# Optimization experiments

Hardware: AMD Instinct MI355X
Metric: run time of the kernel (lower is better)

The kernel has to match this reference:

```python
import jax, jax.numpy as jnp
import numpy as np

TEMP = 100.0          # config.networks.pseudo_temp
THRESH2 = 100.0 ** 2  # config.networks.keypoint_loss.error_thresh ** 2
NEG = -1e30


def se3_inv(T):
    R, t = T[:3, :3], T[:3, 3]
    return jnp.eye(4, dtype=T.dtype).at[:3, :3].set(R.T).at[:3, 3].set(-R.T @ t)


def convert_weight_mat(w):
    # w: [N,6] -> Wmat = L diag(exp(d)) L^T  (unit lower-triangular L), d = w[:,3:6]
    N = w.shape[0]
    d = w[:, 3:6]
    L = jnp.tile(jnp.eye(3, dtype=w.dtype), (N, 1, 1))
    L = L.at[:, 1, 0].set(w[:, 0]).at[:, 2, 0].set(w[:, 1]).at[:, 2, 1].set(w[:, 2])
    Wmat = jnp.einsum('nij,nj,nkj->nik', L, jnp.exp(d), L)
    return Wmat, d


def _pair_loss(src, tgt, w, m1, m2, wv, T_src, T_tgt):
    # src,tgt: [3,N]; w: [6,N]; m1,m2: [N] bool masks (ragged nonzero -> masking); wv: [N,N]
    N = wv.shape[0]
    points1 = src.T                                   # [N,3]
    w12c = jnp.where(m2[None, :], wv, NEG)            # mask invalid tgt columns
    soft = jax.nn.softmax(w12c * TEMP, axis=1)        # pseudo-correspondence weights
    points2 = soft @ tgt.T                            # [N,3] pseudo points
    Wmat, d = convert_weight_mat(w.T)                 # [N,3,3], [N,3]
    # match consistency (argmax in both directions over valid rows/cols)
    ind2to1 = jnp.argmax(w12c, axis=1)
    ind1to2 = jnp.argmax(jnp.where(m1[:, None], wv, NEG), axis=0)
    consist = ind1to2[ind2to1] == jnp.arange(N)
    mask = m1 & consist
    # groundtruth relative transform, transport points1 into frame 2
    T21 = se3_inv(T_tgt) @ T_src
    p1in2 = points1 @ T21[:3, :3].T + T21[:3, 3][None, :]
    e = p1in2 - points2                               # steam_pseudo: points2e == points2
    mah = jnp.einsum('ni,nij,nj->n', e, Wmat, e)      # Mahalanobis error
    inlier = (mask & (mah < THRESH2)).astype(mah.dtype)
    cnt = jnp.maximum(inlier.sum(), 1.0)
    # weighted MSE (mean of e^T W e over inliers) minus mean log-det reward
    return (mah * inlier).sum() / cnt - (d.sum(1) * inlier).sum() / cnt


def setup_inputs() -> dict:
    key = jax.random.key(0)
    ks = jax.random.split(key, 6)
    B, N = 4, 5760
    return {
        'src_coords': jax.random.normal(ks[0], (B, 3, N), jnp.float32),
        'tgt_coords': jax.random.normal(ks[1], (B, 3, N), jnp.float32),
        'weights':    jax.random.normal(ks[2], (B, 6, N), jnp.float32),
        'match_vals': jax.random.normal(ks[3], (B, N, N), jnp.float32),
        'T_iv':       jax.random.normal(ks[4], (2 * B, 4, 4), jnp.float32),
        'patch_mask': jax.random.randint(ks[5], (2 * B, N), 0, 2, jnp.int32),
    }


def reference(src_coords, tgt_coords, weights, match_vals, T_iv, patch_mask):
    m = patch_mask.astype(bool)
    losses = jax.vmap(_pair_loss)(
        src_coords, tgt_coords, weights,
        m[0::2], m[1::2], match_vals, T_iv[0::2], T_iv[1::2])
    return losses.sum()
```

## Files before the change

kernel.cpp:

```cpp
#include <hip/hip_runtime.h>
#include <stdint.h>

#define TEMP_F 100.0f
#define NEG_F (-1e30f)
#define THRESH2_F 10000.0f

typedef unsigned long long ull;

__device__ __forceinline__ ull packvi(float v, int idx) {
    unsigned u = __float_as_uint(v);
    u = (u & 0x80000000u) ? ~u : (u | 0x80000000u);
    return (((ull)u) << 32) | (ull)(0xFFFFFFFFu - (unsigned)idx);
}
__device__ __forceinline__ float unpackv(ull p) {
    unsigned u = (unsigned)(p >> 32);
    u = (u & 0x80000000u) ? (u & 0x7FFFFFFFu) : ~u;
    return __uint_as_float(u);
}
__device__ __forceinline__ ull u64max(ull a, ull b) { return a > b ? a : b; }

__global__ void init_kernel(const float* __restrict__ Tiv,
                            ull* __restrict__ colPacked,
                            float* __restrict__ acc, float* __restrict__ T21,
                            int* __restrict__ validCnt,
                            int B, int N) {
    int idx = blockIdx.x * 256 + threadIdx.x;
    if (idx < B * N) colPacked[idx] = packvi(NEG_F, 0);
    if (idx < B * 3) acc[idx] = 0.0f;
    if (idx < B) validCnt[idx] = 0;
    if (idx < B) {
        const float* Ts = Tiv + (size_t)(2 * idx) * 16;
        const float* Tt = Tiv + (size_t)(2 * idx + 1) * 16;
        float* T = T21 + idx * 12;
        for (int i = 0; i < 3; i++) {
            float mi3 = -(Tt[0 * 4 + i] * Tt[0 * 4 + 3] +
                          Tt[1 * 4 + i] * Tt[1 * 4 + 3] +
                          Tt[2 * 4 + i] * Tt[2 * 4 + 3]);
            for (int j = 0; j < 4; j++) {
                T[i * 4 + j] = Tt[0 * 4 + i] * Ts[0 * 4 + j] +
                               Tt[1 * 4 + i] * Ts[1 * 4 + j] +
                               Tt[2 * 4 + i] * Ts[2 * 4 + j] +
                               mi3 * Ts[3 * 4 + j];
            }
        }
    }
}

__global__ void compact_kernel(const int* __restrict__ pm,
                               int* __restrict__ validRows, int* __restrict__ validCnt,
                               int N) {
    int b = blockIdx.y;
    int i = blockIdx.x * 256 + threadIdx.x;
    if (i < N && pm[(size_t)(2 * b) * N + i]) {
        int pos = atomicAdd(&validCnt[b], 1);
        validRows[(size_t)b * N + pos] = i;
    }
}

__global__ __launch_bounds__(256) void rows_kernel(const float* __restrict__ wv,
                                                   const float* __restrict__ tgt,
                                                   const int* __restrict__ pm,
                                                   float* __restrict__ points2,
                                                   unsigned* __restrict__ ind2to1,
                                                   int N) {
    const int b = blockIdx.y;
    const int i = blockIdx.x;
    const float* row = wv + ((size_t)b * N + i) * N;
    const float* t0 = tgt + (size_t)b * 3 * N;
    const float* t1 = t0 + N;
    const float* t2 = t1 + N;
    const int* m2 = pm + (size_t)(2 * b + 1) * N;
    const int t = threadIdx.x;
    const int N4 = N >> 2;

    __shared__ float xv[5760];
    __shared__ ull sb[256];

    float4* xv4 = (float4*)xv;
    ull best = 0ull;
    for (int j4 = t; j4 < N4; j4 += 256) {
        float4 r = ((const float4*)row)[j4];
        int4 mk = ((const int4*)m2)[j4];
        int j = j4 << 2;
        float v0 = mk.x ? r.x : NEG_F;
        float v1 = mk.y ? r.y : NEG_F;
        float v2 = mk.z ? r.z : NEG_F;
        float v3 = mk.w ? r.w : NEG_F;
        best = u64max(best, u64max(u64max(packvi(v0, j), packvi(v1, j + 1)),
                                   u64max(packvi(v2, j + 2), packvi(v3, j + 3))));
        float4 xs;
        xs.x = TEMP_F * v0; xs.y = TEMP_F * v1; xs.z = TEMP_F * v2; xs.w = TEMP_F * v3;
        xv4[j4] = xs;
    }
    sb[t] = best;
    __syncthreads();
    for (int off = 128; off > 0; off >>= 1) {
        if (t < off) sb[t] = u64max(sb[t], sb[t + off]);
        __syncthreads();
    }
    const ull bfin = sb[0];
    const float M = TEMP_F * unpackv(bfin);
    __syncthreads();

    float s = 0.f, p0 = 0.f, p1 = 0.f, p2 = 0.f;
    for (int j4 = t; j4 < N4; j4 += 256) {
        float4 xs = xv4[j4];
        float w0 = __expf(xs.x - M);
        float w1 = __expf(xs.y - M);
        float w2 = __expf(xs.z - M);
        float w3 = __expf(xs.w - M);
        float4 a = ((const float4*)t0)[j4];
        float4 c = ((const float4*)t1)[j4];
        float4 d = ((const float4*)t2)[j4];
        s += (w0 + w1) + (w2 + w3);
        p0 += (w0 * a.x + w1 * a.y) + (w2 * a.z + w3 * a.w);
        p1 += (w0 * c.x + w1 * c.y) + (w2 * c.z + w3 * c.w);
        p2 += (w0 * d.x + w1 * d.y) + (w2 * d.z + w3 * d.w);
    }
    __syncthreads();
    float* rs = xv;
    rs[t] = s; rs[256 + t] = p0; rs[512 + t] = p1; rs[768 + t] = p2;
    __syncthreads();
    for (int off = 128; off > 0; off >>= 1) {
        if (t < off) {
            rs[t] += rs[t + off];
            rs[256 + t] += rs[256 + t + off];
            rs[512 + t] += rs[512 + t + off];
            rs[768 + t] += rs[768 + t + off];
        }
        __syncthreads();
    }
    if (t == 0) {
        float inv = 1.0f / rs[0];
        size_t o = ((size_t)b * N + i) * 3;
        points2[o + 0] = rs[256] * inv;
        points2[o + 1] = rs[512] * inv;
        points2[o + 2] = rs[768] * inv;
        ind2to1[(size_t)b * N + i] = 0xFFFFFFFFu - (unsigned)(bfin & 0xFFFFFFFFull);
    }
}

__global__ __launch_bounds__(256) void cols_kernel(const float* __restrict__ wv,
                                                   const int* __restrict__ validRows,
                                                   const int* __restrict__ validCnt,
                                                   ull* __restrict__ colPacked,
                                                   int N, int S) {
    const int b = blockIdx.z;
    const int col = blockIdx.x * 256 + threadIdx.x;
    if (col >= N) return;
    const int cnt = validCnt[b];
    const int per = (cnt + S - 1) / S;
    int k0 = blockIdx.y * per;
    int k1 = k0 + per; if (k1 > cnt) k1 = cnt;
    const int* vr = validRows + (size_t)b * N;
    const float* base = wv + (size_t)b * N * N + col;

    ull best = 0ull;
    int k = k0;
    for (; k + 8 <= k1; k += 8) {
        int i0 = vr[k + 0], i1 = vr[k + 1], i2 = vr[k + 2], i3 = vr[k + 3];
        int i4 = vr[k + 4], i5 = vr[k + 5], i6 = vr[k + 6], i7 = vr[k + 7];
        float v0 = base[(size_t)i0 * N];
        float v1 = base[(size_t)i1 * N];
        float v2 = base[(size_t)i2 * N];
        float v3 = base[(size_t)i3 * N];
        float v4 = base[(size_t)i4 * N];
        float v5 = base[(size_t)i5 * N];
        float v6 = base[(size_t)i6 * N];
        float v7 = base[(size_t)i7 * N];
        ull b0 = u64max(packvi(v0, i0), packvi(v1, i1));
        ull b1 = u64max(packvi(v2, i2), packvi(v3, i3));
        ull b2 = u64max(packvi(v4, i4), packvi(v5, i5));
        ull b3 = u64max(packvi(v6, i6), packvi(v7, i7));
        best = u64max(best, u64max(u64max(b0, b1), u64max(b2, b3)));
    }
    for (; k < k1; k++) {
        int i0 = vr[k];
        best = u64max(best, packvi(base[(size_t)i0 * N], i0));
    }
    if (best) atomicMax(&colPacked[(size_t)b * N + col], best);
}

__global__ __launch_bounds__(256) void loss_kernel(const float* __restrict__ src,
                                                   const float* __restrict__ wts,
                                                   const int* __restrict__ pm,
                                                   const float* __restrict__ points2,
                                                   const unsigned* __restrict__ ind2to1,
                                                   const ull* __restrict__ colPacked,
                                                   const float* __restrict__ T21,
                                                   float* __restrict__ acc, int N) {
    const int b = blockIdx.y;
    const int i = blockIdx.x * 256 + threadIdx.x;
    float lm = 0.f, ld = 0.f, lc = 0.f;
    if (i < N) {
        const int* m1 = pm + (size_t)(2 * b) * N;
        bool msk = (m1[i] != 0);
        unsigned j = ind2to1[(size_t)b * N + i];
        unsigned i2 = 0xFFFFFFFFu - (unsigned)(colPacked[(size_t)b * N + j] & 0xFFFFFFFFull);
        bool consist = (i2 == (unsigned)i);
        const float* T = T21 + b * 12;
        const float* s0 = src + (size_t)b * 3 * N;
        float x = s0[i], y = s0[N + i], z = s0[2 * (size_t)N + i];
        size_t o = ((size_t)b * N + i) * 3;
        float e0 = T[0] * x + T[1] * y + T[2]  * z + T[3]  - points2[o + 0];
        float e1 = T[4] * x + T[5] * y + T[6]  * z + T[7]  - points2[o + 1];
        float e2 = T[8] * x + T[9] * y + T[10] * z + T[11] - points2[o + 2];
        const float* w = wts + (size_t)b * 6 * N;
        float a  = w[i];
        float bb = w[N + i];
        float c  = w[2 * (size_t)N + i];
        float d0 = w[3 * (size_t)N + i];
        float d1 = w[4 * (size_t)N + i];
        float d2 = w[5 * (size_t)N + i];
        float u0 = e0 + a * e1 + bb * e2;
        float u1 = e1 + c * e2;
        float u2 = e2;
        float mah = expf(d0) * u0 * u0 + expf(d1) * u1 * u1 + expf(d2) * u2 * u2;
        if (msk && consist && (mah < THRESH2_F)) {
            lm = mah; ld = d0 + d1 + d2; lc = 1.0f;
        }
    }
    __shared__ float r0[256], r1[256], r2[256];
    const int t = threadIdx.x;
    r0[t] = lm; r1[t] = ld; r2[t] = lc;
    __syncthreads();
    for (int off = 128; off > 0; off >>= 1) {
        if (t < off) { r0[t] += r0[t + off]; r1[t] += r1[t + off]; r2[t] += r2[t + off]; }
        __syncthreads();
    }
    if (t == 0) {
        atomicAdd(&acc[b * 3 + 0], r0[0]);
        atomicAdd(&acc[b * 3 + 1], r1[0]);
        atomicAdd(&acc[b * 3 + 2], r2[0]);
    }
}

__global__ void finish_kernel(const float* __restrict__ acc, float* __restrict__ out, int B) {
    if (threadIdx.x == 0 && blockIdx.x == 0) {
        float total = 0.f;
        for (int b = 0; b < B; b++) {
            float cnt = fmaxf(acc[b * 3 + 2], 1.0f);
            total += (acc[b * 3 + 0] - acc[b * 3 + 1]) / cnt;
        }
        out[0] = total;
    }
}

extern "C" void kernel_launch(void* const* d_in, const int* in_sizes, int n_in,
                              void* d_out, int out_size, void* d_ws, size_t ws_size,
                              hipStream_t stream) {
    const float* src = (const float*)d_in[0];
    const float* tgt = (const float*)d_in[1];
    const float* wts = (const float*)d_in[2];
    const float* wv  = (const float*)d_in[3];
    const float* Tiv = (const float*)d_in[4];
    const int*   pm  = (const int*)d_in[5];
    float* out = (float*)d_out;

    long long s0 = in_sizes[0], s3 = in_sizes[3];
    int N = (int)(3LL * s3 / s0);
    int B = (int)(s0 / (3LL * (long long)N));

    char* w = (char*)d_ws;
    ull* colPacked = (ull*)w;        w += sizeof(ull) * (size_t)B * N;
    float* points2 = (float*)w;      w += sizeof(float) * (size_t)B * N * 3;
    unsigned* ind2to1 = (unsigned*)w; w += sizeof(unsigned) * (size_t)B * N;
    int* validRows = (int*)w;        w += sizeof(int) * (size_t)B * N;
    int* validCnt = (int*)w;         w += sizeof(int) * (size_t)B;
    float* T21 = (float*)w;          w += sizeof(float) * (size_t)B * 12;
    float* acc = (float*)w;          w += sizeof(float) * (size_t)B * 3;

    int nb = (N + 255) / 256;
    init_kernel<<<(B * N + 255) / 256, 256, 0, stream>>>(Tiv, colPacked, acc, T21, validCnt, B, N);
    compact_kernel<<<dim3(nb, B), 256, 0, stream>>>(pm, validRows, validCnt, N);

    dim3 gRows(N, B);
    rows_kernel<<<gRows, 256, 0, stream>>>(wv, tgt, pm, points2, ind2to1, N);

    const int S = 8;
    dim3 gCols(nb, S, B);
    cols_kernel<<<gCols, 256, 0, stream>>>(wv, validRows, validCnt, colPacked, N, S);

    dim3 gLoss(nb, B);
    loss_kernel<<<gLoss, 256, 0, stream>>>(src, wts, pm, points2, ind2to1, colPacked, T21, acc, N);

    finish_kernel<<<1, 64, 0, stream>>>(acc, out, B);
}
```

Measured before the change: 795.5 us.

## Fuse row softmax and column argmax into one single-pass kernel over valid rows

Replaces the separate rows and cols kernels with one kernel that reads each valid row of the match matrix once. It computes an online softmax (running max and rescaled sums) per wave and keeps per-block column maxima in shared memory using LDS atomics, which are then flushed to global with atomicMax. Rows whose m1 mask is off are skipped, since their softmax results are never used. This aims to remove the second full pass over the large matrix and the strided column reads. The cost is heavy LDS atomic traffic and extra exp work from the online rescaling.

```diff
diff --git a/kernel.cpp b/kernel.cpp
--- a/kernel.cpp
+++ b/kernel.cpp
@@ -3,6 +3,7 @@
 
 #define TEMP_F 100.0f
 #define NEG_F (-1e30f)
+#define XNEG_F (-1e32f)
 #define THRESH2_F 10000.0f
 
 typedef unsigned long long ull;
@@ -11,11 +12,6 @@
     unsigned u = __float_as_uint(v);
     u = (u & 0x80000000u) ? ~u : (u | 0x80000000u);
     return (((ull)u) << 32) | (ull)(0xFFFFFFFFu - (unsigned)idx);
-}
-__device__ __forceinline__ float unpackv(ull p) {
-    unsigned u = (unsigned)(p >> 32);
-    u = (u & 0x80000000u) ? (u & 0x7FFFFFFFu) : ~u;
-    return __uint_as_float(u);
 }
 __device__ __forceinline__ ull u64max(ull a, ull b) { return a > b ? a : b; }
 
@@ -57,135 +53,126 @@
     }
 }
 
-__global__ __launch_bounds__(256) void rows_kernel(const float* __restrict__ wv,
-                                                   const float* __restrict__ tgt,
-                                                   const int* __restrict__ pm,
-                                                   float* __restrict__ points2,
-                                                   unsigned* __restrict__ ind2to1,
-                                                   int N) {
+__global__ __launch_bounds__(512, 4) void fused_kernel(const float* __restrict__ wv,
+                                                       const float* __restrict__ tgt,
+                                                       const int* __restrict__ pm,
+                                                       const int* __restrict__ validRows,
+                                                       const int* __restrict__ validCnt,
+                                                       ull* __restrict__ colPacked,
+                                                       float4* __restrict__ points2raw,
+                                                       int* __restrict__ ind2to1,
+                                                       int N) {
+    __shared__ ull colmax[5760];
     const int b = blockIdx.y;
-    const int i = blockIdx.x;
-    const float* row = wv + ((size_t)b * N + i) * N;
+    const int tid = threadIdx.x;
+    const int N4 = N >> 2;
+
+    for (int j = tid; j < N; j += 512) colmax[j] = 0ull;
+    __syncthreads();
+
+    const int lane = tid & 63;
+    const int wave = tid >> 6;
+    const int W = gridDim.x * 8;
+    const int wg = blockIdx.x * 8 + wave;
+    const int cnt = validCnt[b];
+    const int* vr = validRows + (size_t)b * N;
+    const int* m2p = pm + (size_t)(2 * b + 1) * N;
     const float* t0 = tgt + (size_t)b * 3 * N;
     const float* t1 = t0 + N;
     const float* t2 = t1 + N;
-    const int* m2 = pm + (size_t)(2 * b + 1) * N;
-    const int t = threadIdx.x;
-    const int N4 = N >> 2;
-
-    __shared__ float xv[5760];
-    __shared__ ull sb[256];
-
-    float4* xv4 = (float4*)xv;
-    ull best = 0ull;
-    for (int j4 = t; j4 < N4; j4 += 256) {
-        float4 r = ((const float4*)row)[j4];
-        int4 mk = ((const int4*)m2)[j4];
-        int j = j4 << 2;
-        float v0 = mk.x ? r.x : NEG_F;
-        float v1 = mk.y ? r.y : NEG_F;
-        float v2 = mk.z ? r.z : NEG_F;
-        float v3 = mk.w ? r.w : NEG_F;
-        best = u64max(best, u64max(u64max(packvi(v0, j), packvi(v1, j + 1)),
-                                   u64max(packvi(v2, j + 2), packvi(v3, j + 3))));
-        float4 xs;
-        xs.x = TEMP_F * v0; xs.y = TEMP_F * v1; xs.z = TEMP_F * v2; xs.w = TEMP_F * v3;
-        xv4[j4] = xs;
-    }
-    sb[t] = best;
+
+    for (int k = wg; k < cnt; k += W) {
+        const int i = vr[k];
+        const float* row = wv + ((size_t)b * N + i) * N;
+
+        float mA[4], sA[4], p0A[4], p1A[4], p2A[4], bv[4];
+        int bi[4];
+        #pragma unroll
+        for (int q = 0; q < 4; q++) {
+            mA[q] = -INFINITY; sA[q] = 0.f; p0A[q] = 0.f; p1A[q] = 0.f; p2A[q] = 0.f;
+            bv[q] = -INFINITY; bi[q] = 0;
+        }
+
+        for (int j4 = lane; j4 < N4; j4 += 64) {
+            float4 r  = ((const float4*)row)[j4];
+            int4  mk  = ((const int4*)m2p)[j4];
+            float4 a0 = ((const float4*)t0)[j4];
+            float4 a1 = ((const float4*)t1)[j4];
+            float4 a2 = ((const float4*)t2)[j4];
+            const int j = j4 << 2;
+            float rr[4] = {r.x, r.y, r.z, r.w};
+            int   mm[4] = {mk.x, mk.y, mk.z, mk.w};
+            float u0[4] = {a0.x, a0.y, a0.z, a0.w};
+            float u1[4] = {a1.x, a1.y, a1.z, a1.w};
+            float u2[4] = {a2.x, a2.y, a2.z, a2.w};
+            #pragma unroll
+            for (int q = 0; q < 4; q++) {
+                float rv = rr[q];
+                atomicMax(&colmax[q * N4 + j4], packvi(rv, i));
+                float x = mm[q] ? (TEMP_F * rv) : XNEG_F;
+                if (x > bv[q]) { bv[q] = x; bi[q] = j + q; }
+                float mn = fmaxf(mA[q], x);
+                float sc = __expf(mA[q] - mn);
+                float w  = __expf(x - mn);
+                sA[q]  = fmaf(sA[q],  sc, w);
+                p0A[q] = fmaf(p0A[q], sc, w * u0[q]);
+                p1A[q] = fmaf(p1A[q], sc, w * u1[q]);
+                p2A[q] = fmaf(p2A[q], sc, w * u2[q]);
+                mA[q] = mn;
+            }
+        }
+
+        float M = mA[0], S = sA[0], P0 = p0A[0], P1 = p1A[0], P2 = p2A[0];
+        float BV = bv[0]; int BI = bi[0];
+        #pragma unroll
+        for (int q = 1; q < 4; q++) {
+            float mn = fmaxf(M, mA[q]);
+            float e1 = __expf(M - mn), e2 = __expf(mA[q] - mn);
+            S  = S  * e1 + sA[q]  * e2;
+            P0 = P0 * e1 + p0A[q] * e2;
+            P1 = P1 * e1 + p1A[q] * e2;
+            P2 = P2 * e1 + p2A[q] * e2;
+            M = mn;
+            if (bv[q] > BV || (bv[q] == BV && bi[q] < BI)) { BV = bv[q]; BI = bi[q]; }
+        }
+        for (int off = 32; off > 0; off >>= 1) {
+            float Mo  = __shfl_xor(M,  off);
+            float So  = __shfl_xor(S,  off);
+            float P0o = __shfl_xor(P0, off);
+            float P1o = __shfl_xor(P1, off);
+            float P2o = __shfl_xor(P2, off);
+            float BVo = __shfl_xor(BV, off);
+            int   BIo = __shfl_xor(BI, off);
+            float mn = fmaxf(M, Mo);
+            float e1 = __expf(M - mn), e2 = __expf(Mo - mn);
+            S  = S  * e1 + So  * e2;
+            P0 = P0 * e1 + P0o * e2;
+            P1 = P1 * e1 + P1o * e2;
+            P2 = P2 * e1 + P2o * e2;
+            M = mn;
+            if (BVo > BV || (BVo == BV && BIo < BI)) { BV = BVo; BI = BIo; }
+        }
+        if (lane == 0) {
+            points2raw[(size_t)b * N + i] = make_float4(P0, P1, P2, S);
+            ind2to1[(size_t)b * N + i] = BI;
+        }
+    }
+
     __syncthreads();
-    for (int off = 128; off > 0; off >>= 1) {
-        if (t < off) sb[t] = u64max(sb[t], sb[t + off]);
-        __syncthreads();
-    }
-    const ull bfin = sb[0];
-    const float M = TEMP_F * unpackv(bfin);
-    __syncthreads();
-
-    float s = 0.f, p0 = 0.f, p1 = 0.f, p2 = 0.f;
-    for (int j4 = t; j4 < N4; j4 += 256) {
-        float4 xs = xv4[j4];
-        float w0 = __expf(xs.x - M);
-        float w1 = __expf(xs.y - M);
-        float w2 = __expf(xs.z - M);
-        float w3 = __expf(xs.w - M);
-        float4 a = ((const float4*)t0)[j4];
-        float4 c = ((const float4*)t1)[j4];
-        float4 d = ((const float4*)t2)[j4];
-        s += (w0 + w1) + (w2 + w3);
-        p0 += (w0 * a.x + w1 * a.y) + (w2 * a.z + w3 * a.w);
-        p1 += (w0 * c.x + w1 * c.y) + (w2 * c.z + w3 * c.w);
-        p2 += (w0 * d.x + w1 * d.y) + (w2 * d.z + w3 * d.w);
-    }
-    __syncthreads();
-    float* rs = xv;
-    rs[t] = s; rs[256 + t] = p0; rs[512 + t] = p1; rs[768 + t] = p2;
-    __syncthreads();
-    for (int off = 128; off > 0; off >>= 1) {
-        if (t < off) {
-            rs[t] += rs[t + off];
-            rs[256 + t] += rs[256 + t + off];
-            rs[512 + t] += rs[512 + t + off];
-            rs[768 + t] += rs[768 + t + off];
-        }
-        __syncthreads();
-    }
-    if (t == 0) {
-        float inv = 1.0f / rs[0];
-        size_t o = ((size_t)b * N + i) * 3;
-        points2[o + 0] = rs[256] * inv;
-        points2[o + 1] = rs[512] * inv;
-        points2[o + 2] = rs[768] * inv;
-        ind2to1[(size_t)b * N + i] = 0xFFFFFFFFu - (unsigned)(bfin & 0xFFFFFFFFull);
-    }
-}
-
-__global__ __launch_bounds__(256) void cols_kernel(const float* __restrict__ wv,
-                                                   const int* __restrict__ validRows,
-                                                   const int* __restrict__ validCnt,
-                                                   ull* __restrict__ colPacked,
-                                                   int N, int S) {
-    const int b = blockIdx.z;
-    const int col = blockIdx.x * 256 + threadIdx.x;
-    if (col >= N) return;
-    const int cnt = validCnt[b];
-    const int per = (cnt + S - 1) / S;
-    int k0 = blockIdx.y * per;
-    int k1 = k0 + per; if (k1 > cnt) k1 = cnt;
-    const int* vr = validRows + (size_t)b * N;
-    const float* base = wv + (size_t)b * N * N + col;
-
-    ull best = 0ull;
-    int k = k0;
-    for (; k + 8 <= k1; k += 8) {
-        int i0 = vr[k + 0], i1 = vr[k + 1], i2 = vr[k + 2], i3 = vr[k + 3];
-        int i4 = vr[k + 4], i5 = vr[k + 5], i6 = vr[k + 6], i7 = vr[k + 7];
-        float v0 = base[(size_t)i0 * N];
-        float v1 = base[(size_t)i1 * N];
-        float v2 = base[(size_t)i2 * N];
-        float v3 = base[(size_t)i3 * N];
-        float v4 = base[(size_t)i4 * N];
-        float v5 = base[(size_t)i5 * N];
-        float v6 = base[(size_t)i6 * N];
-        float v7 = base[(size_t)i7 * N];
-        ull b0 = u64max(packvi(v0, i0), packvi(v1, i1));
-        ull b1 = u64max(packvi(v2, i2), packvi(v3, i3));
-        ull b2 = u64max(packvi(v4, i4), packvi(v5, i5));
-        ull b3 = u64max(packvi(v6, i6), packvi(v7, i7));
-        best = u64max(best, u64max(u64max(b0, b1), u64max(b2, b3)));
-    }
-    for (; k < k1; k++) {
-        int i0 = vr[k];
-        best = u64max(best, packvi(base[(size_t)i0 * N], i0));
-    }
-    if (best) atomicMax(&colPacked[(size_t)b * N + col], best);
+    for (int t = tid; t < N; t += 512) {
+        ull v = colmax[t];
+        if (v) {
+            int j = ((t % N4) << 2) | (t / N4);
+            atomicMax(&colPacked[(size_t)b * N + j], v);
+        }
+    }
 }
 
 __global__ __launch_bounds__(256) void loss_kernel(const float* __restrict__ src,
                                                    const float* __restrict__ wts,
                                                    const int* __restrict__ pm,
-                                                   const float* __restrict__ points2,
-                                                   const unsigned* __restrict__ ind2to1,
+                                                   const float4* __restrict__ points2raw,
+                                                   const int* __restrict__ ind2to1,
                                                    const ull* __restrict__ colPacked,
                                                    const float* __restrict__ T21,
                                                    float* __restrict__ acc, int N) {
@@ -195,16 +182,17 @@
     if (i < N) {
         const int* m1 = pm + (size_t)(2 * b) * N;
         bool msk = (m1[i] != 0);
-        unsigned j = ind2to1[(size_t)b * N + i];
+        int j = msk ? ind2to1[(size_t)b * N + i] : 0;
         unsigned i2 = 0xFFFFFFFFu - (unsigned)(colPacked[(size_t)b * N + j] & 0xFFFFFFFFull);
-        bool consist = (i2 == (unsigned)i);
+        bool consist = ((int)i2 == i);
         const float* T = T21 + b * 12;
         const float* s0 = src + (size_t)b * 3 * N;
         float x = s0[i], y = s0[N + i], z = s0[2 * (size_t)N + i];
-        size_t o = ((size_t)b * N + i) * 3;
-        float e0 = T[0] * x + T[1] * y + T[2]  * z + T[3]  - points2[o + 0];
-        float e1 = T[4] * x + T[5] * y + T[6]  * z + T[7]  - points2[o + 1];
-        float e2 = T[8] * x + T[9] * y + T[10] * z + T[11] - points2[o + 2];
+        float4 pr = points2raw[(size_t)b * N + i];
+        float inv = 1.0f / pr.w;
+        float e0 = T[0] * x + T[1] * y + T[2]  * z + T[3]  - pr.x * inv;
+        float e1 = T[4] * x + T[5] * y + T[6]  * z + T[7]  - pr.y * inv;
+        float e2 = T[8] * x + T[9] * y + T[10] * z + T[11] - pr.z * inv;
         const float* w = wts + (size_t)b * 6 * N;
         float a  = w[i];
         float bb = w[N + i];
@@ -212,10 +200,10 @@
         float d0 = w[3 * (size_t)N + i];
         float d1 = w[4 * (size_t)N + i];
         float d2 = w[5 * (size_t)N + i];
-        float u0 = e0 + a * e1 + bb * e2;
-        float u1 = e1 + c * e2;
-        float u2 = e2;
-        float mah = expf(d0) * u0 * u0 + expf(d1) * u1 * u1 + expf(d2) * u2 * u2;
+        float v0 = e0 + a * e1 + bb * e2;
+        float v1 = e1 + c * e2;
+        float v2 = e2;
+        float mah = expf(d0) * v0 * v0 + expf(d1) * v1 * v1 + expf(d2) * v2 * v2;
         if (msk && consist && (mah < THRESH2_F)) {
             lm = mah; ld = d0 + d1 + d2; lc = 1.0f;
         }
@@ -262,27 +250,24 @@
     int B = (int)(s0 / (3LL * (long long)N));
 
     char* w = (char*)d_ws;
-    ull* colPacked = (ull*)w;        w += sizeof(ull) * (size_t)B * N;
-    float* points2 = (float*)w;      w += sizeof(float) * (size_t)B * N * 3;
-    unsigned* ind2to1 = (unsigned*)w; w += sizeof(unsigned) * (size_t)B * N;
-    int* validRows = (int*)w;        w += sizeof(int) * (size_t)B * N;
-    int* validCnt = (int*)w;         w += sizeof(int) * (size_t)B;
-    float* T21 = (float*)w;          w += sizeof(float) * (size_t)B * 12;
-    float* acc = (float*)w;          w += sizeof(float) * (size_t)B * 3;
+    ull* colPacked = (ull*)w;         w += sizeof(ull) * (size_t)B * N;
+    float4* points2raw = (float4*)w;  w += sizeof(float4) * (size_t)B * N;
+    int* ind2to1 = (int*)w;           w += sizeof(int) * (size_t)B * N;
+    int* validRows = (int*)w;         w += sizeof(int) * (size_t)B * N;
+    int* validCnt = (int*)w;          w += sizeof(int) * (size_t)B;
+    float* T21 = (float*)w;           w += sizeof(float) * (size_t)B * 12;
+    float* acc = (float*)w;           w += sizeof(float) * (size_t)B * 3;
 
     int nb = (N + 255) / 256;
     init_kernel<<<(B * N + 255) / 256, 256, 0, stream>>>(Tiv, colPacked, acc, T21, validCnt, B, N);
     compact_kernel<<<dim3(nb, B), 256, 0, stream>>>(pm, validRows, validCnt, N);
 
-    dim3 gRows(N, B);
-    rows_kernel<<<gRows, 256, 0, stream>>>(wv, tgt, pm, points2, ind2to1, N);
-
-    const int S = 8;
-    dim3 gCols(nb, S, B);
-    cols_kernel<<<gCols, 256, 0, stream>>>(wv, validRows, validCnt, colPacked, N, S);
+    dim3 gF(128, B);
+    fused_kernel<<<gF, 512, 0, stream>>>(wv, tgt, pm, validRows, validCnt,
+                                         colPacked, points2raw, ind2to1, N);
 
     dim3 gLoss(nb, B);
-    loss_kernel<<<gLoss, 256, 0, stream>>>(src, wts, pm, points2, ind2to1, colPacked, T21, acc, N);
+    loss_kernel<<<gLoss, 256, 0, stream>>>(src, wts, pm, points2raw, ind2to1, colPacked, T21, acc, N);
 
     finish_kernel<<<1, 64, 0, stream>>>(acc, out, B);
 }
```

New measurement: 710.8 us. 10.6% less time.
